# Performance work log

Measured on AMD Instinct MI355X. Metric: run time of the kernel, lower is better.

The kernel has to match this reference:

```python
import jax, jax.numpy as jnp
import numpy as np

B, T, D = 2, 2048, 1024
H, HD = 16, 64
DL, DC = 512, 256
THETA = 10000.0
LN_EPS = 1e-5


def setup_inputs() -> dict:
    key = jax.random.key(0)
    ks = jax.random.split(key, 8)
    s = 0.02
    return {
        "x": jax.random.normal(ks[0], (B, T, D), jnp.float32),
        "W_q": jax.random.normal(ks[1], (H * HD, D), jnp.float32) * s,
        "b_q": jnp.zeros((H * HD,), jnp.float32),
        "W_kvl": jax.random.normal(ks[2], (DL, D), jnp.float32) * s,
        "b_kvl": jnp.zeros((DL,), jnp.float32),
        "ts_scale": jnp.ones((DL,), jnp.float32),
        "ts_shift": jnp.zeros((DL,), jnp.float32),
        "W_comp": jax.random.normal(ks[3], (DC, DL), jnp.float32) * s,
        "W_exp": jax.random.normal(ks[4], (DL, DC), jnp.float32) * s,
        "ln_g": jnp.ones((DC,), jnp.float32),
        "ln_b": jnp.zeros((DC,), jnp.float32),
        "W_fkv": jax.random.normal(ks[5], (2 * H * HD, DL), jnp.float32) * s,
        "b_fkv": jnp.zeros((2 * H * HD,), jnp.float32),
        "W_out": jax.random.normal(ks[6], (D, H * HD), jnp.float32) * s,
        "b_out": jnp.zeros((D,), jnp.float32),
    }


def _rope_tables(t_len):
    inv_freq = 1.0 / (THETA ** (jnp.arange(0, HD, 2, dtype=jnp.float32) / HD))
    pos = jnp.arange(t_len, dtype=jnp.float32)
    freqs = pos[:, None] * inv_freq[None, :]          # [T, HD/2]
    cos = jnp.concatenate([jnp.cos(freqs)] * 2, -1)   # [T, HD]
    sin = jnp.concatenate([jnp.sin(freqs)] * 2, -1)
    return cos[None, None], sin[None, None]           # [1,1,T,HD]


def _rotate_half(z):
    return jnp.concatenate([-z[..., HD // 2:], z[..., :HD // 2]], -1)


def reference(x, W_q, b_q, W_kvl, b_kvl, ts_scale, ts_shift, W_comp, W_exp,
              ln_g, ln_b, W_fkv, b_fkv, W_out, b_out):
    # Q path: [B,T,D] -> [B,H,T,HD]
    q = (jnp.einsum('btd,ed->bte', x, W_q) + b_q).reshape(B, T, H, HD).transpose(0, 2, 1, 3)

    # KV latent + learned KVSplice bottleneck
    kvl = jnp.einsum('btd,ld->btl', x, W_kvl) + b_kvl                 # [B,T,DL]
    xt = kvl * jax.nn.softplus(ts_scale) + ts_shift
    c = jnp.einsum('btl,cl->btc', xt, W_comp)                         # [B,T,DC]
    mu = jnp.mean(c, -1, keepdims=True)
    var = jnp.mean(jnp.square(c - mu), -1, keepdims=True)
    c = (c - mu) * jax.lax.rsqrt(var + LN_EPS) * ln_g + ln_b
    dec = jnp.einsum('btc,lc->btl', c, W_exp)                         # [B,T,DL]

    # Decompress latent to K,V
    kv = jnp.einsum('btl,el->bte', dec, W_fkv) + b_fkv                # [B,T,2*H*HD]
    kv = kv.reshape(B, T, 2, H, HD).transpose(2, 0, 3, 1, 4)          # [2,B,H,T,HD]
    k, v = kv[0], kv[1]

    # RoPE
    cos, sin = _rope_tables(T)
    q = q * cos + _rotate_half(q) * sin
    k = k * cos + _rotate_half(k) * sin

    # Causal SDPA
    scale = 1.0 / np.sqrt(HD)
    scores = jnp.einsum('bhqd,bhkd->bhqk', q, k) * scale
    mask = jnp.tril(jnp.ones((T, T), bool))
    scores = jnp.where(mask, scores, jnp.float32(-1e30))
    attn = jax.nn.softmax(scores, axis=-1)
    o = jnp.einsum('bhqk,bhkd->bhqd', attn, v)
    o = o.transpose(0, 2, 1, 3).reshape(B, T, H * HD)
    return jnp.einsum('bte,de->btd', o, W_out) + b_out
```

## Files before the change

kernel.cpp:

```cpp
#include <hip/hip_runtime.h>
#include <math.h>

#define B_SZ   2
#define T_SEQ  2048
#define NH     16
#define HDIM   64
#define D_MOD  1024
#define DL     512
#define DC     256
#define MROWS  4096

typedef __attribute__((ext_vector_type(8))) short bf16x8;
typedef __attribute__((ext_vector_type(4))) float f32x4;

#define SCALE_Q 0.18033688011112042f

static __device__ __forceinline__ unsigned short f2bf(float f) {
    union { float f; unsigned u; } v; v.f = f;
    unsigned r = v.u + 0x7fffu + ((v.u >> 16) & 1u);
    return (unsigned short)(r >> 16);
}

static __device__ __forceinline__ void gl_lds16(const unsigned short* g,
                                                unsigned short* l) {
    __builtin_amdgcn_global_load_lds(
        (const __attribute__((address_space(1))) unsigned int*)g,
        (__attribute__((address_space(3))) unsigned int*)l, 16, 0, 0);
}

__global__ __launch_bounds__(256) void cvt_bf16(
    const float* __restrict__ x,  const float* __restrict__ wq,
    const float* __restrict__ wkvl, const float* __restrict__ wcomp,
    const float* __restrict__ wexp, const float* __restrict__ wfkv,
    const float* __restrict__ wout,
    unsigned short* __restrict__ xb,  unsigned short* __restrict__ wqh,
    unsigned short* __restrict__ wkvlh, unsigned short* __restrict__ wcomph,
    unsigned short* __restrict__ wexph, unsigned short* __restrict__ wfkvh,
    unsigned short* __restrict__ wouth, float2* __restrict__ rope_tab)
{
    const int g = blockIdx.x * 256 + threadIdx.x;
    const int stride = gridDim.x * 256;
#define CVT_SEG(src, dst, n4)                                              \
    for (int i = g; i < (n4); i += stride) {                               \
        float4 v = ((const float4*)(src))[i];                              \
        unsigned short h[4] = {f2bf(v.x), f2bf(v.y), f2bf(v.z), f2bf(v.w)};\
        *(uint2*)((dst) + (size_t)i * 4) = *(uint2*)h;                     \
    }
    CVT_SEG(x, xb, 1048576)
    CVT_SEG(wq, wqh, 262144)
    CVT_SEG(wkvl, wkvlh, 131072)
    CVT_SEG(wcomp, wcomph, 32768)
    CVT_SEG(wexp, wexph, 32768)
    CVT_SEG(wfkv, wfkvh, 262144)
    CVT_SEG(wout, wouth, 262144)
#undef CVT_SEG
    for (int i = g; i < T_SEQ * 32; i += stride) {
        const int t = i >> 5, fi = i & 31;
        const float inv = __expf((float)fi * (-9.210340371976184f / 32.0f));
        float sn, cs; sincosf((float)t * inv, &sn, &cs);
        rope_tab[i] = make_float2(cs, sn);
    }
}

#define GEMM64R_PROLOG(Aptr, Wptr, Kdim)                                       \
    __shared__ unsigned short As[64 * 32];                                     \
    __shared__ unsigned short Ws[64 * 32];                                     \
    const int tid = threadIdx.x;                                               \
    const int w = tid >> 6, lane = tid & 63;                                   \
    const int l16 = lane & 15, quad = lane >> 4;                               \
    const int srow = lane >> 2, scol = (lane & 3) << 3;                        \
    const unsigned short* Ag = (Aptr) + (size_t)(m0 + w * 16 + srow) * (Kdim) + scol; \
    const unsigned short* Wg = (Wptr) + (size_t)(n0 + w * 16 + srow) * (Kdim) + scol; \
    unsigned short* Al = &As[w * 512];                                         \
    unsigned short* Wl = &Ws[w * 512];                                         \
    f32x4 acc[4];                                                              \
    _Pragma("unroll") for (int j = 0; j < 4; ++j)                              \
        acc[j] = (f32x4){0.f, 0.f, 0.f, 0.f};                                  \
    for (int k0 = 0; k0 < (Kdim); k0 += 32) {                                  \
        __syncthreads();                                                       \
        gl_lds16(Ag + k0, Al);                                                 \
        gl_lds16(Wg + k0, Wl);                                                 \
        __syncthreads();                                                       \
        const bf16x8 af = *(const bf16x8*)&As[(w * 16 + l16) * 32 + quad * 8]; \
        bf16x8 bfr[4];                                                         \
        _Pragma("unroll") for (int j = 0; j < 4; ++j)                          \
            bfr[j] = *(const bf16x8*)&Ws[(j * 16 + l16) * 32 + quad * 8];      \
        _Pragma("unroll") for (int j = 0; j < 4; ++j)                          \
            acc[j] = __builtin_amdgcn_mfma_f32_16x16x32_bf16(af, bfr[j], acc[j], 0, 0, 0); \
    }

__global__ __launch_bounds__(256) void gemm_qxt(
    const unsigned short* __restrict__ A, const unsigned short* __restrict__ Wq,
    const unsigned short* __restrict__ Wkvl,
    const float* __restrict__ b_q, const float* __restrict__ b_kvl,
    const float* __restrict__ ts_scale, const float* __restrict__ ts_shift,
    const float2* __restrict__ tab,
    unsigned short* __restrict__ qh, unsigned short* __restrict__ xt)
{
    const int m0 = blockIdx.x * 64;
    const bool is_q = (blockIdx.y < 16);
    const int n0 = is_q ? blockIdx.y * 64 : (blockIdx.y - 16) * 64;
    const unsigned short* W = is_q ? Wq : Wkvl;

    GEMM64R_PROLOG(A, W, D_MOD)

    if (is_q) {
#pragma unroll
        for (int j = 0; j < 4; ++j) {
            const int col = n0 + j * 16 + l16;
            const int h = col >> 6, hd = col & 63;
            const float bv = b_q[col];
            const float bvp = b_q[col ^ 32];
            const float sgn = (hd < 32) ? -1.f : 1.f;
#pragma unroll
            for (int reg = 0; reg < 4; ++reg) {
                const int row = m0 + w * 16 + quad * 4 + reg;
                const int b = row >> 11, t = row & (T_SEQ - 1);
                const float2 cssn = tab[t * 32 + (hd & 31)];
                const float v  = acc[j][reg] + bv;
                const float vp = acc[j ^ 2][reg] + bvp;
                const float r = (v * cssn.x + sgn * vp * cssn.y) * SCALE_Q;
                qh[(((size_t)b * NH + h) * T_SEQ + t) * HDIM + hd] = f2bf(r);
            }
        }
    } else {
#pragma unroll
        for (int j = 0; j < 4; ++j) {
            const int col = n0 + j * 16 + l16;
            const float bv = b_kvl[col];
            const float sp_s = log1pf(expf(ts_scale[col]));
            const float sp_t = ts_shift[col];
#pragma unroll
            for (int reg = 0; reg < 4; ++reg) {
                const int row = m0 + w * 16 + quad * 4 + reg;
                const float val = (acc[j][reg] + bv) * sp_s + sp_t;
                xt[(size_t)row * DL + col] = f2bf(val);
            }
        }
    }
}

__global__ __launch_bounds__(256) void gemm_kv(
    const unsigned short* __restrict__ A, const unsigned short* __restrict__ W,
    const float* __restrict__ bias, const float2* __restrict__ tab,
    unsigned short* __restrict__ kh, unsigned short* __restrict__ vth)
{
    const int m0 = blockIdx.x * 64, n0 = blockIdx.y * 64;

    GEMM64R_PROLOG(A, W, DL)

    if (n0 < 1024) {
#pragma unroll
        for (int j = 0; j < 4; ++j) {
            const int col = n0 + j * 16 + l16;
            const int h = (col >> 6) & 15, hd = col & 63;
            const float bv = bias[col];
            const float bvp = bias[col ^ 32];
            const float sgn = (hd < 32) ? -1.f : 1.f;
#pragma unroll
            for (int reg = 0; reg < 4; ++reg) {
                const int row = m0 + w * 16 + quad * 4 + reg;
                const int b = row >> 11, t = row & (T_SEQ - 1);
                const float2 cssn = tab[t * 32 + (hd & 31)];
                const float v  = acc[j][reg] + bv;
                const float vp = acc[j ^ 2][reg] + bvp;
                const float r = v * cssn.x + sgn * vp * cssn.y;
                kh[(((size_t)b * NH + h) * T_SEQ + t) * HDIM + hd] = f2bf(r);
            }
        }
    } else {
#pragma unroll
        for (int j = 0; j < 4; ++j) {
            const int col = n0 + j * 16 + l16;
            const int cv = col - 1024;
            const int h = cv >> 6, hd = cv & 63;
            const float bv = bias[col];
            unsigned short hv[4];
            const int r0 = m0 + w * 16 + quad * 4;
            const int b = r0 >> 11, t0 = r0 & (T_SEQ - 1);
#pragma unroll
            for (int reg = 0; reg < 4; ++reg)
                hv[reg] = f2bf(acc[j][reg] + bv);
            *(uint2*)&vth[(((size_t)b * NH + h) * HDIM + hd) * T_SEQ + t0] =
                *(uint2*)hv;
        }
    }
}

__global__ __launch_bounds__(256) void gemm_out(
    const unsigned short* __restrict__ A, const unsigned short* __restrict__ W,
    const float* __restrict__ bias, float* __restrict__ C)
{
    const int m0 = blockIdx.x * 64, n0 = blockIdx.y * 64;

    GEMM64R_PROLOG(A, W, D_MOD)

#pragma unroll
    for (int j = 0; j < 4; ++j) {
        const int col = n0 + j * 16 + l16;
        const float bv = bias[col];
#pragma unroll
        for (int reg = 0; reg < 4; ++reg) {
            const int row = m0 + w * 16 + quad * 4 + reg;
            C[(size_t)row * D_MOD + col] = acc[j][reg] + bv;
        }
    }
}

__global__ __launch_bounds__(256) void gemm_c_ln(
    const unsigned short* __restrict__ A, const unsigned short* __restrict__ W,
    const float* __restrict__ g, const float* __restrict__ bta,
    unsigned short* __restrict__ outb)
{
    __shared__ unsigned short As[16 * 32];
    __shared__ unsigned short Ws[256 * 32];
    __shared__ float redS[4][16];
    __shared__ float redQ[4][16];

    const int tid = threadIdx.x;
    const int w = tid >> 6, lane = tid & 63;
    const int l16 = lane & 15, quad = lane >> 4;
    const int m0 = blockIdx.x * 16;

    const int srow = lane >> 2, scol = (lane & 3) << 3;
    const unsigned short* Ag = A + (size_t)(m0 + srow) * DL + scol;
    const unsigned short* Wg = W + (size_t)(w * 64 + srow) * DL + scol;

    f32x4 acc[4];
#pragma unroll
    for (int j = 0; j < 4; ++j) acc[j] = (f32x4){0.f, 0.f, 0.f, 0.f};

    for (int k0 = 0; k0 < DL; k0 += 32) {
        __syncthreads();
        if (w == 0) gl_lds16(Ag + k0, &As[0]);
#pragma unroll
        for (int c = 0; c < 4; ++c)
            gl_lds16(Wg + (size_t)(c * 16) * DL + k0, &Ws[(w * 64 + c * 16) * 32]);
        __syncthreads();

        const bf16x8 af = *(const bf16x8*)&As[l16 * 32 + quad * 8];
        bf16x8 bfr[4];
#pragma unroll
        for (int j = 0; j < 4; ++j)
            bfr[j] = *(const bf16x8*)&Ws[(w * 64 + j * 16 + l16) * 32 + quad * 8];
#pragma unroll
        for (int j = 0; j < 4; ++j)
            acc[j] = __builtin_amdgcn_mfma_f32_16x16x32_bf16(af, bfr[j], acc[j], 0, 0, 0);
    }

    float s[4], q2[4];
#pragma unroll
    for (int reg = 0; reg < 4; ++reg) {
        float sv = (acc[0][reg] + acc[1][reg]) + (acc[2][reg] + acc[3][reg]);
        float qv = (acc[0][reg] * acc[0][reg] + acc[1][reg] * acc[1][reg]) +
                   (acc[2][reg] * acc[2][reg] + acc[3][reg] * acc[3][reg]);
#pragma unroll
        for (int off = 1; off < 16; off <<= 1) {
            sv += __shfl_xor(sv, off);
            qv += __shfl_xor(qv, off);
        }
        s[reg] = sv; q2[reg] = qv;
    }
    if (l16 == 0) {
#pragma unroll
        for (int reg = 0; reg < 4; ++reg) {
            redS[w][quad * 4 + reg] = s[reg];
            redQ[w][quad * 4 + reg] = q2[reg];
        }
    }
    __syncthreads();

#pragma unroll
    for (int reg = 0; reg < 4; ++reg) {
        const int r = quad * 4 + reg;
        const float sum = (redS[0][r] + redS[1][r]) + (redS[2][r] + redS[3][r]);
        const float sq  = (redQ[0][r] + redQ[1][r]) + (redQ[2][r] + redQ[3][r]);
        const float mu  = sum * (1.0f / DC);
        const float var = sq * (1.0f / DC) - mu * mu;
        const float rstd = rsqrtf(var + 1e-5f);
#pragma unroll
        for (int j = 0; j < 4; ++j) {
            const int col = w * 64 + j * 16 + l16;
            const float val = (acc[j][reg] - mu) * rstd * g[col] + bta[col];
            outb[(size_t)(m0 + r) * DC + col] = f2bf(val);
        }
    }
}

__global__ __launch_bounds__(256) void gemm_mfma64_b(
    const unsigned short* __restrict__ A, const unsigned short* __restrict__ W,
    unsigned short* __restrict__ Cv, int N, int K)
{
    __shared__ unsigned short As[64 * 32];
    __shared__ unsigned short Ws[64 * 32];

    const int tid = threadIdx.x;
    const int w = tid >> 6, lane = tid & 63;
    const int l16 = lane & 15, quad = lane >> 4;
    const int wm = w >> 1, wn = w & 1;
    const int m0 = blockIdx.x * 64, n0 = blockIdx.y * 64;

    const unsigned short* Ag = A + (size_t)(m0 + w * 16 + (lane >> 2)) * K + ((lane & 3) << 3);
    const unsigned short* Wg = W + (size_t)(n0 + w * 16 + (lane >> 2)) * K + ((lane & 3) << 3);
    unsigned short* Al = &As[w * 512];
    unsigned short* Wl = &Ws[w * 512];

    f32x4 acc[2][2];
#pragma unroll
    for (int i = 0; i < 2; ++i)
#pragma unroll
        for (int j = 0; j < 2; ++j) acc[i][j] = (f32x4){0.f, 0.f, 0.f, 0.f};

    for (int k0 = 0; k0 < K; k0 += 32) {
        __syncthreads();
        gl_lds16(Ag + k0, Al);
        gl_lds16(Wg + k0, Wl);
        __syncthreads();

        bf16x8 af[2], bfr[2];
#pragma unroll
        for (int i = 0; i < 2; ++i)
            af[i] = *(const bf16x8*)&As[(wm * 32 + i * 16 + l16) * 32 + quad * 8];
#pragma unroll
        for (int j = 0; j < 2; ++j)
            bfr[j] = *(const bf16x8*)&Ws[(wn * 32 + j * 16 + l16) * 32 + quad * 8];
#pragma unroll
        for (int i = 0; i < 2; ++i)
#pragma unroll
            for (int j = 0; j < 2; ++j)
                acc[i][j] = __builtin_amdgcn_mfma_f32_16x16x32_bf16(
                    af[i], bfr[j], acc[i][j], 0, 0, 0);
    }

#pragma unroll
    for (int i = 0; i < 2; ++i) {
#pragma unroll
        for (int j = 0; j < 2; ++j) {
            const int col = n0 + wn * 32 + j * 16 + l16;
#pragma unroll
            for (int reg = 0; reg < 4; ++reg) {
                const int row = m0 + wm * 32 + i * 16 + quad * 4 + reg;
                Cv[(size_t)row * N + col] = f2bf(acc[i][j][reg]);
            }
        }
    }
}

__global__ __launch_bounds__(256, 3) void flash_mfma(
    const unsigned short* __restrict__ q, const unsigned short* __restrict__ k,
    const unsigned short* __restrict__ vt, unsigned short* __restrict__ o)
{
    __shared__ unsigned short Ks[64 * 72];
    __shared__ unsigned short Vs[64 * 72];
    __shared__ unsigned short Ps[64 * 72];

    const int bh = blockIdx.x & 31;
    const int j  = 31 - (blockIdx.x >> 5);
    const int q0 = j * 64;
    const int tid = threadIdx.x;
    const int w = tid >> 6, lane = tid & 63;
    const int l16 = lane & 15, quad = lane >> 4;
    const int rbase = q0 + w * 16;

    bf16x8 qf[2];
#pragma unroll
    for (int kk = 0; kk < 2; ++kk)
        qf[kk] = *(const bf16x8*)(q + ((size_t)bh * T_SEQ + rbase + l16) * HDIM + kk * 32 + quad * 8);

    f32x4 of[4];
    float lrow[4];
#pragma unroll
    for (int dt = 0; dt < 4; ++dt) of[dt] = (f32x4){0.f, 0.f, 0.f, 0.f};
#pragma unroll
    for (int r = 0; r < 4; ++r) lrow[r] = 0.f;

    const int ldr = tid >> 2;
    const int ldc = (tid & 3) * 16;
    const unsigned short* kgb = k + ((size_t)bh * T_SEQ + ldr) * HDIM + ldc;
    const unsigned short* vgb = vt + ((size_t)bh * HDIM + ldr) * T_SEQ + ldc;

    const int kend = (j + 1) * 64;
    for (int k0 = 0; k0 < kend; k0 += 64) {
        __syncthreads();
        {
            const unsigned short* kg = kgb + (size_t)k0 * HDIM;
            *(bf16x8*)&Ks[ldr * 72 + ldc]     = *(const bf16x8*)kg;
            *(bf16x8*)&Ks[ldr * 72 + ldc + 8] = *(const bf16x8*)(kg + 8);
            const unsigned short* vg = vgb + k0;
            *(bf16x8*)&Vs[ldr * 72 + ldc]     = *(const bf16x8*)vg;
            *(bf16x8*)&Vs[ldr * 72 + ldc + 8] = *(const bf16x8*)(vg + 8);
        }
        __syncthreads();

        bf16x8 kf[4][2];
#pragma unroll
        for (int nt = 0; nt < 4; ++nt)
#pragma unroll
            for (int kk = 0; kk < 2; ++kk)
                kf[nt][kk] = *(const bf16x8*)&Ks[(nt * 16 + l16) * 72 + kk * 32 + quad * 8];

        f32x4 sf[4];
#pragma unroll
        for (int nt = 0; nt < 4; ++nt) {
            sf[nt] = (f32x4){0.f, 0.f, 0.f, 0.f};
#pragma unroll
            for (int kk = 0; kk < 2; ++kk)
                sf[nt] = __builtin_amdgcn_mfma_f32_16x16x32_bf16(qf[kk], kf[nt][kk], sf[nt], 0, 0, 0);
        }

        const bool need_mask = (k0 + 63) > rbase;
#pragma unroll
        for (int reg = 0; reg < 4; ++reg) {
            float a0 = sf[0][reg], a1 = sf[1][reg], a2 = sf[2][reg], a3 = sf[3][reg];
            if (need_mask) {
                const int tq = rbase + quad * 4 + reg;
                if (k0 +      l16 > tq) a0 = -1e30f;
                if (k0 + 16 + l16 > tq) a1 = -1e30f;
                if (k0 + 32 + l16 > tq) a2 = -1e30f;
                if (k0 + 48 + l16 > tq) a3 = -1e30f;
            }
            union { float f; unsigned u; } u0, u1, u2, u3;
            u0.f = exp2f(a0); u1.f = exp2f(a1);
            u2.f = exp2f(a2); u3.f = exp2f(a3);
            const int prow = (w * 16 + quad * 4 + reg) * 72 + l16;
            Ps[prow]      = (unsigned short)(u0.u >> 16);
            Ps[prow + 16] = (unsigned short)(u1.u >> 16);
            Ps[prow + 32] = (unsigned short)(u2.u >> 16);
            Ps[prow + 48] = (unsigned short)(u3.u >> 16);
            u0.u &= 0xffff0000u; u1.u &= 0xffff0000u;
            u2.u &= 0xffff0000u; u3.u &= 0xffff0000u;
            lrow[reg] += (u0.f + u1.f) + (u2.f + u3.f);
        }

        bf16x8 vf[4][2];
#pragma unroll
        for (int dt = 0; dt < 4; ++dt)
#pragma unroll
            for (int kk = 0; kk < 2; ++kk)
                vf[dt][kk] = *(const bf16x8*)&Vs[(dt * 16 + l16) * 72 + kk * 32 + quad * 8];

        bf16x8 pf[2];
#pragma unroll
        for (int kk = 0; kk < 2; ++kk)
            pf[kk] = *(const bf16x8*)&Ps[(w * 16 + l16) * 72 + kk * 32 + quad * 8];
#pragma unroll
        for (int dt = 0; dt < 4; ++dt)
#pragma unroll
            for (int kk = 0; kk < 2; ++kk)
                of[dt] = __builtin_amdgcn_mfma_f32_16x16x32_bf16(pf[kk], vf[dt][kk], of[dt], 0, 0, 0);
    }

    const int b = bh >> 4, h = bh & 15;
#pragma unroll
    for (int reg = 0; reg < 4; ++reg) {
        float l = lrow[reg];
        l += __shfl_xor(l, 1);
        l += __shfl_xor(l, 2);
        l += __shfl_xor(l, 4);
        l += __shfl_xor(l, 8);
        const float inv = 1.0f / l;
        const int t = rbase + quad * 4 + reg;
#pragma unroll
        for (int dt = 0; dt < 4; ++dt)
            o[((size_t)b * T_SEQ + t) * (NH * HDIM) + h * HDIM + dt * 16 + l16] =
                f2bf(of[dt][reg] * inv);
    }
}

extern "C" void kernel_launch(void* const* d_in, const int* in_sizes, int n_in,
                              void* d_out, int out_size, void* d_ws, size_t ws_size,
                              hipStream_t stream)
{
    (void)in_sizes; (void)n_in; (void)out_size; (void)ws_size;

    const float* x        = (const float*)d_in[0];
    const float* W_q      = (const float*)d_in[1];
    const float* b_q      = (const float*)d_in[2];
    const float* W_kvl    = (const float*)d_in[3];
    const float* b_kvl    = (const float*)d_in[4];
    const float* ts_scale = (const float*)d_in[5];
    const float* ts_shift = (const float*)d_in[6];
    const float* W_comp   = (const float*)d_in[7];
    const float* W_exp    = (const float*)d_in[8];
    const float* ln_g     = (const float*)d_in[9];
    const float* ln_b     = (const float*)d_in[10];
    const float* W_fkv    = (const float*)d_in[11];
    const float* b_fkv    = (const float*)d_in[12];
    const float* W_out    = (const float*)d_in[13];
    const float* b_out    = (const float*)d_in[14];
    float* out = (float*)d_out;

    char* p = (char*)d_ws;
    unsigned short* xb     = (unsigned short*)p;             p += 8  * 1024 * 1024;
    unsigned short* wqh    = (unsigned short*)p;             p += 2  * 1024 * 1024;
    unsigned short* wkvlh  = (unsigned short*)p;             p += 1  * 1024 * 1024;
    unsigned short* wcomph = (unsigned short*)p;             p += 256 * 1024;
    unsigned short* wexph  = (unsigned short*)p;             p += 256 * 1024;
    unsigned short* wfkvh  = (unsigned short*)p;             p += 2  * 1024 * 1024;
    unsigned short* wouth  = (unsigned short*)p;             p += 2  * 1024 * 1024;
    unsigned short* qh     = (unsigned short*)p;             p += 8  * 1024 * 1024;
    unsigned short* kh     = (unsigned short*)p;             p += 8  * 1024 * 1024;
    unsigned short* vth    = (unsigned short*)p;             p += 8  * 1024 * 1024;
    unsigned short* xt     = (unsigned short*)p;             p += 4  * 1024 * 1024;
    unsigned short* cbh    = (unsigned short*)p;             p += 2  * 1024 * 1024;
    unsigned short* dec    = (unsigned short*)p;             p += 4  * 1024 * 1024;
    unsigned short* ob     = (unsigned short*)p;             p += 8  * 1024 * 1024;
    float2*         tab    = (float2*)p;                     p += 512 * 1024;

    const dim3 blk(256);

    cvt_bf16<<<1024, blk, 0, stream>>>(x, W_q, W_kvl, W_comp, W_exp, W_fkv, W_out,
                                       xb, wqh, wkvlh, wcomph, wexph, wfkvh, wouth,
                                       tab);

    gemm_qxt<<<dim3(64, 24), blk, 0, stream>>>(
        xb, wqh, wkvlh, b_q, b_kvl, ts_scale, ts_shift, tab, qh, xt);

    gemm_c_ln<<<256, blk, 0, stream>>>(
        xt, wcomph, ln_g, ln_b, cbh);

    gemm_mfma64_b<<<dim3(64, 8), blk, 0, stream>>>(
        cbh, wexph, dec, DL, DC);

    gemm_kv<<<dim3(64, 32), blk, 0, stream>>>(
        dec, wfkvh, b_fkv, tab, kh, vth);

    flash_mfma<<<1024, blk, 0, stream>>>(qh, kh, vth, ob);

    gemm_out<<<dim3(64, 16), blk, 0, stream>>>(
        ob, wouth, b_out, out);
}
```

Before: 240.9 us.

## Fuse LayerNorm output into expansion GEMM and retune P tile stride

The compress+LayerNorm kernel now keeps its normalized 16x256 tile in LDS and directly multiplies it by W_exp, writing the decompressed latent. This removes one kernel launch and the global round trip of the intermediate normalized tensor. The trade-off is that the expansion GEMM runs on only 256 blocks and streams W_exp straight from global memory without LDS reuse. Separately, the flash-attention P buffer row stride changes from 72 to 68 to alter its LDS bank mapping.

After: 250.0 us. +3.8%, slower.

```diff
diff --git a/kernel.cpp b/kernel.cpp
--- a/kernel.cpp
+++ b/kernel.cpp
@@ -14,6 +14,7 @@
 typedef __attribute__((ext_vector_type(4))) float f32x4;
 
 #define SCALE_Q 0.18033688011112042f
+#define PSTR 68
 
 static __device__ __forceinline__ unsigned short f2bf(float f) {
     union { float f; unsigned u; } v; v.f = f;
@@ -207,13 +208,15 @@
     }
 }
 
-__global__ __launch_bounds__(256) void gemm_c_ln(
-    const unsigned short* __restrict__ A, const unsigned short* __restrict__ W,
+__global__ __launch_bounds__(256) void gemm_cb(
+    const unsigned short* __restrict__ A, const unsigned short* __restrict__ Wc,
+    const unsigned short* __restrict__ We,
     const float* __restrict__ g, const float* __restrict__ bta,
-    unsigned short* __restrict__ outb)
+    unsigned short* __restrict__ dec)
 {
     __shared__ unsigned short As[16 * 32];
     __shared__ unsigned short Ws[256 * 32];
+    __shared__ unsigned short Cs[16 * 260];
     __shared__ float redS[4][16];
     __shared__ float redQ[4][16];
 
@@ -224,7 +227,7 @@
 
     const int srow = lane >> 2, scol = (lane & 3) << 3;
     const unsigned short* Ag = A + (size_t)(m0 + srow) * DL + scol;
-    const unsigned short* Wg = W + (size_t)(w * 64 + srow) * DL + scol;
+    const unsigned short* Wg = Wc + (size_t)(w * 64 + srow) * DL + scol;
 
     f32x4 acc[4];
 #pragma unroll
@@ -282,67 +285,29 @@
         for (int j = 0; j < 4; ++j) {
             const int col = w * 64 + j * 16 + l16;
             const float val = (acc[j][reg] - mu) * rstd * g[col] + bta[col];
-            outb[(size_t)(m0 + r) * DC + col] = f2bf(val);
-        }
-    }
-}
-
-__global__ __launch_bounds__(256) void gemm_mfma64_b(
-    const unsigned short* __restrict__ A, const unsigned short* __restrict__ W,
-    unsigned short* __restrict__ Cv, int N, int K)
-{
-    __shared__ unsigned short As[64 * 32];
-    __shared__ unsigned short Ws[64 * 32];
-
-    const int tid = threadIdx.x;
-    const int w = tid >> 6, lane = tid & 63;
-    const int l16 = lane & 15, quad = lane >> 4;
-    const int wm = w >> 1, wn = w & 1;
-    const int m0 = blockIdx.x * 64, n0 = blockIdx.y * 64;
-
-    const unsigned short* Ag = A + (size_t)(m0 + w * 16 + (lane >> 2)) * K + ((lane & 3) << 3);
-    const unsigned short* Wg = W + (size_t)(n0 + w * 16 + (lane >> 2)) * K + ((lane & 3) << 3);
-    unsigned short* Al = &As[w * 512];
-    unsigned short* Wl = &Ws[w * 512];
-
-    f32x4 acc[2][2];
-#pragma unroll
-    for (int i = 0; i < 2; ++i)
-#pragma unroll
-        for (int j = 0; j < 2; ++j) acc[i][j] = (f32x4){0.f, 0.f, 0.f, 0.f};
-
-    for (int k0 = 0; k0 < K; k0 += 32) {
-        __syncthreads();
-        gl_lds16(Ag + k0, Al);
-        gl_lds16(Wg + k0, Wl);
-        __syncthreads();
-
-        bf16x8 af[2], bfr[2];
-#pragma unroll
-        for (int i = 0; i < 2; ++i)
-            af[i] = *(const bf16x8*)&As[(wm * 32 + i * 16 + l16) * 32 + quad * 8];
-#pragma unroll
-        for (int j = 0; j < 2; ++j)
-            bfr[j] = *(const bf16x8*)&Ws[(wn * 32 + j * 16 + l16) * 32 + quad * 8];
-#pragma unroll
-        for (int i = 0; i < 2; ++i)
-#pragma unroll
-            for (int j = 0; j < 2; ++j)
-                acc[i][j] = __builtin_amdgcn_mfma_f32_16x16x32_bf16(
-                    af[i], bfr[j], acc[i][j], 0, 0, 0);
-    }
-
-#pragma unroll
-    for (int i = 0; i < 2; ++i) {
-#pragma unroll
-        for (int j = 0; j < 2; ++j) {
-            const int col = n0 + wn * 32 + j * 16 + l16;
-#pragma unroll
-            for (int reg = 0; reg < 4; ++reg) {
-                const int row = m0 + wm * 32 + i * 16 + quad * 4 + reg;
-                Cv[(size_t)row * N + col] = f2bf(acc[i][j][reg]);
-            }
-        }
+            Cs[r * 260 + col] = f2bf(val);
+        }
+    }
+    __syncthreads();
+
+    bf16x8 a2[8];
+#pragma unroll
+    for (int kk = 0; kk < 8; ++kk)
+        a2[kk] = *(const bf16x8*)&Cs[l16 * 260 + kk * 32 + quad * 8];
+
+#pragma unroll
+    for (int j = 0; j < 8; ++j) {
+        f32x4 acc2 = (f32x4){0.f, 0.f, 0.f, 0.f};
+        const unsigned short* Bg = We + (size_t)(w * 128 + j * 16 + l16) * DC + quad * 8;
+#pragma unroll
+        for (int kk = 0; kk < 8; ++kk) {
+            const bf16x8 b2 = *(const bf16x8*)(Bg + kk * 32);
+            acc2 = __builtin_amdgcn_mfma_f32_16x16x32_bf16(a2[kk], b2, acc2, 0, 0, 0);
+        }
+        const int col = w * 128 + j * 16 + l16;
+#pragma unroll
+        for (int reg = 0; reg < 4; ++reg)
+            dec[(size_t)(m0 + quad * 4 + reg) * DL + col] = f2bf(acc2[reg]);
     }
 }
 
@@ -352,7 +317,7 @@
 {
     __shared__ unsigned short Ks[64 * 72];
     __shared__ unsigned short Vs[64 * 72];
-    __shared__ unsigned short Ps[64 * 72];
+    __shared__ unsigned short Ps[64 * PSTR];
 
     const int bh = blockIdx.x & 31;
     const int j  = 31 - (blockIdx.x >> 5);
@@ -422,7 +387,7 @@
             union { float f; unsigned u; } u0, u1, u2, u3;
             u0.f = exp2f(a0); u1.f = exp2f(a1);
             u2.f = exp2f(a2); u3.f = exp2f(a3);
-            const int prow = (w * 16 + quad * 4 + reg) * 72 + l16;
+            const int prow = (w * 16 + quad * 4 + reg) * PSTR + l16;
             Ps[prow]      = (unsigned short)(u0.u >> 16);
             Ps[prow + 16] = (unsigned short)(u1.u >> 16);
             Ps[prow + 32] = (unsigned short)(u2.u >> 16);
@@ -442,7 +407,7 @@
         bf16x8 pf[2];
 #pragma unroll
         for (int kk = 0; kk < 2; ++kk)
-            pf[kk] = *(const bf16x8*)&Ps[(w * 16 + l16) * 72 + kk * 32 + quad * 8];
+            pf[kk] = *(const bf16x8*)&Ps[(w * 16 + l16) * PSTR + kk * 32 + quad * 8];
 #pragma unroll
         for (int dt = 0; dt < 4; ++dt)
 #pragma unroll
@@ -502,7 +467,6 @@
     unsigned short* kh     = (unsigned short*)p;             p += 8  * 1024 * 1024;
     unsigned short* vth    = (unsigned short*)p;             p += 8  * 1024 * 1024;
     unsigned short* xt     = (unsigned short*)p;             p += 4  * 1024 * 1024;
-    unsigned short* cbh    = (unsigned short*)p;             p += 2  * 1024 * 1024;
     unsigned short* dec    = (unsigned short*)p;             p += 4  * 1024 * 1024;
     unsigned short* ob     = (unsigned short*)p;             p += 8  * 1024 * 1024;
     float2*         tab    = (float2*)p;                     p += 512 * 1024;
@@ -516,11 +480,8 @@
     gemm_qxt<<<dim3(64, 24), blk, 0, stream>>>(
         xb, wqh, wkvlh, b_q, b_kvl, ts_scale, ts_shift, tab, qh, xt);
 
-    gemm_c_ln<<<256, blk, 0, stream>>>(
-        xt, wcomph, ln_g, ln_b, cbh);
-
-    gemm_mfma64_b<<<dim3(64, 8), blk, 0, stream>>>(
-        cbh, wexph, dec, DL, DC);
+    gemm_cb<<<256, blk, 0, stream>>>(
+        xt, wcomph, wexph, ln_g, ln_b, dec);
 
     gemm_kv<<<dim3(64, 32), blk, 0, stream>>>(
         dec, wfkvh, b_fkv, tab, kh, vth);
```
